# Kernel tuning notes

Hardware: AMD Instinct MI355X
Metric: run time of the kernel (lower is better)

Reference implementation:

```python
import jax, jax.numpy as jnp
import numpy as np

VOCAB = 32000
N = 4096        # reservoir_size
D = 32          # avg nonzeros per row -> density D/N
R_OUT = 512
BATCH = 8
T = 256
NNZ = N * D     # W_rec nonzeros = N*N*(D/N)


def setup_inputs() -> dict:
    key = jax.random.key(0)
    ks = jax.random.split(key, 9)
    x = jax.random.randint(ks[0], (BATCH, T), 0, VOCAB)
    # dense input table; sparse.mm(W_in_T, one_hot) == row gather W_in[x_t]
    W_in = jax.random.normal(ks[1], (VOCAB, N), jnp.float32)
    rec_rows = jax.random.randint(ks[2], (NNZ,), 0, N, dtype=jnp.int32)
    rec_cols = jax.random.randint(ks[3], (NNZ,), 0, N, dtype=jnp.int32)
    # small scale stands in for spectral-radius normalization (init-time detail)
    rec_vals = jax.random.normal(ks[4], (NNZ,), jnp.float32) * 0.05
    a = jax.random.uniform(ks[5], (N,), jnp.float32)  # leak rates in [0,1)
    B_w = jax.random.normal(ks[6], (R_OUT, N), jnp.float32) / np.sqrt(N)
    A_w = jax.random.normal(ks[7], (VOCAB, R_OUT), jnp.float32) / np.sqrt(R_OUT)
    A_b = jnp.zeros((VOCAB,), jnp.float32)
    return dict(x=x, W_in=W_in, rec_rows=rec_rows, rec_cols=rec_cols,
                rec_vals=rec_vals, a=a, B_w=B_w, A_w=A_w, A_b=A_b)


def reference(x, W_in, rec_rows, rec_cols, rec_vals, a, B_w, A_w, A_b):
    B = x.shape[0]

    def step(h, x_t):
        # input projection: one-hot @ W_in  ==  row gather
        u = W_in[x_t]                                   # (B, N)
        # sparse COO matvec: rec = W_rec @ h^T, batched over B
        contrib = rec_vals[None, :] * h[:, rec_cols]    # (B, nnz)
        rec = jnp.zeros_like(h).at[:, rec_rows].add(contrib)
        pre = jnp.clip(u + rec, -10.0, 10.0)
        h_new = (1.0 - a) * h + a * jnp.tanh(pre)
        out = (h_new @ B_w.T) @ A_w.T + A_b             # (B, vocab)
        return h_new, out

    h0 = jnp.zeros((B, W_in.shape[1]), W_in.dtype)
    _, outs = jax.lax.scan(step, h0, x.T)               # (T, B, V)
    return jnp.transpose(outs, (1, 0, 2))               # (B, T, V)
```

## Files before the change

### kernel.cpp

```cpp
#include <hip/hip_runtime.h>
#include <hip/hip_bf16.h>
#include <stdint.h>

#define N_RES 4096
#define BATCH 8
#define T_STEPS 256
#define VOCAB 32000
#define R_OUT 512
#define NNZ 131072
#define NNZ_CAP 163840
#define TEAMS 8
#define SLICES 16
#define ROWS_PS 256
#define NWG (TEAMS*SLICES)
#define CSR_CAP 10240

typedef _Float16 v8h __attribute__((ext_vector_type(8)));
typedef float v4f __attribute__((ext_vector_type(4)));

static __device__ __forceinline__ unsigned short f2h(float f) {
    _Float16 h = (_Float16)f;
    unsigned short u;
    __builtin_memcpy(&u, &h, 2);
    return u;
}
static __device__ __forceinline__ float h2f(unsigned short u) {
    _Float16 h;
    __builtin_memcpy(&h, &u, 2);
    return (float)h;
}


__global__ __launch_bounds__(256) void k_zero(unsigned* p, int n) {
    int i = blockIdx.x * 256 + threadIdx.x;
    if (i < n) p[i] = 0u;
}

__global__ __launch_bounds__(256) void k_hist(const int* __restrict__ rows,
                                              int* __restrict__ cnt) {
    int i = blockIdx.x * 256 + threadIdx.x;
    if (i < NNZ) atomicAdd(&cnt[rows[i]], 1);
}

__global__ __launch_bounds__(1024) void k_scan(const int* __restrict__ cnt,
                                               int* __restrict__ row_ptr,
                                               int* __restrict__ cursor) {
    __shared__ int sm[1024];
    int t = threadIdx.x;
    int base = t * 4;
    int c0 = (cnt[base] + 7) & ~7;
    int c1 = (cnt[base + 1] + 7) & ~7;
    int c2 = (cnt[base + 2] + 7) & ~7;
    int c3 = (cnt[base + 3] + 7) & ~7;
    int s = c0 + c1 + c2 + c3;
    sm[t] = s;
    __syncthreads();
    for (int off = 1; off < 1024; off <<= 1) {
        int v = (t >= off) ? sm[t - off] : 0;
        __syncthreads();
        sm[t] += v;
        __syncthreads();
    }
    int run = sm[t] - s;
    row_ptr[base] = run;     cursor[base] = run;     run += c0;
    row_ptr[base + 1] = run; cursor[base + 1] = run; run += c1;
    row_ptr[base + 2] = run; cursor[base + 2] = run; run += c2;
    row_ptr[base + 3] = run; cursor[base + 3] = run; run += c3;
    if (t == 1023) row_ptr[4096] = run;
}

__global__ __launch_bounds__(256) void k_fill(const int* __restrict__ rows,
                                              const int* __restrict__ cols,
                                              const float* __restrict__ vals,
                                              int* __restrict__ cursor,
                                              unsigned* __restrict__ csr) {
    int i = blockIdx.x * 256 + threadIdx.x;
    if (i < NNZ) {
        int r = rows[i];
        int c = cols[i];
        int p = atomicAdd(&cursor[r], 1);
        unsigned off = ((unsigned)(c & 15) << 10) | ((unsigned)(c >> 4) << 2);
        csr[p] = (off << 16) | (unsigned)f2h(vals[i]);
    }
}


__global__ __launch_bounds__(256) void k_cvt(const float* __restrict__ src,
                                             unsigned short* __restrict__ dst, int n) {
    int i = (blockIdx.x * 256 + threadIdx.x) * 8;
    if (i < n) {
        float4 a0 = *reinterpret_cast<const float4*>(src + i);
        float4 a1 = *reinterpret_cast<const float4*>(src + i + 4);
        unsigned short o[8] = { f2h(a0.x), f2h(a0.y), f2h(a0.z), f2h(a0.w),
                                f2h(a1.x), f2h(a1.y), f2h(a1.z), f2h(a1.w) };
        *reinterpret_cast<uint4*>(dst + i) = *reinterpret_cast<const uint4*>(o);
    }
}


__global__ __launch_bounds__(256) void k_steps(const int* __restrict__ rowptr,
                                               const unsigned* __restrict__ csr,
                                               const float* __restrict__ W_in,
                                               const int* __restrict__ x,
                                               const float* __restrict__ a,
                                               unsigned short* __restrict__ Hb,
                                               unsigned long long* __restrict__ hx,
                                               unsigned* __restrict__ flags) {
    __shared__ float plane[4096];
    __shared__ __align__(16) unsigned lcsr[CSR_CAP];
    __shared__ unsigned long long stage64[64];
    __shared__ int ltok[T_STEPS];

    int wg = blockIdx.x;
    int tid = threadIdx.x;
    int team = wg & 7;
    int slice = wg >> 3;
    int r_own = slice * ROWS_PS + tid;

    ltok[tid] = x[team * T_STEPS + tid];

    int j0 = rowptr[slice * ROWS_PS];
    int j1 = rowptr[slice * ROWS_PS + ROWS_PS];
    int cntE = j1 - j0;
    if (cntE > CSR_CAP) cntE = CSR_CAP;
    {
        const uint4* src = reinterpret_cast<const uint4*>(csr + j0);
        int n4 = cntE >> 2;
        for (int k = tid; k < n4; k += 256)
            reinterpret_cast<uint4*>(lcsr)[k] = src[k];
    }
    for (int k = tid; k < 4096; k += 256) plane[k] = 0.f;

    int js = rowptr[r_own] - j0;
    int je = rowptr[r_own + 1] - j0;
    if (js > CSR_CAP) js = CSR_CAP;
    if (je > CSR_CAP) je = CSR_CAP;
    float av = a[r_own];
    float oma = 1.f - av;
    int pown = ((r_own & 15) << 8) | (r_own >> 4);
    __syncthreads();

    float u_cur = W_in[(size_t)ltok[0] * N_RES + r_own];

    for (int t = 0; t < T_STEPS; ++t) {
        float u_nxt = 0.f;
        if (t + 1 < T_STEPS)
            u_nxt = W_in[(size_t)ltok[t + 1] * N_RES + r_own];

        float acc = 0.f;
        for (int j = js; j < je; j += 8) {
            uint4 e0 = *reinterpret_cast<const uint4*>(lcsr + j);
            uint4 e1 = *reinterpret_cast<const uint4*>(lcsr + j + 4);
            unsigned ee[8] = { e0.x, e0.y, e0.z, e0.w, e1.x, e1.y, e1.z, e1.w };
#pragma unroll
            for (int q = 0; q < 8; ++q) {
                float g = *reinterpret_cast<const float*>(
                    reinterpret_cast<const char*>(plane) + (ee[q] >> 16));
                acc += h2f((unsigned short)(ee[q] & 0xffffu)) * g;
            }
        }
        float hold = plane[pown];
        float pre = u_cur + acc;
        pre = fminf(fmaxf(pre, -10.f), 10.f);
        float ex = __expf(2.f * pre);
        float th = 1.f - 2.f / (ex + 1.f);
        float hv = oma * hold + av * th;
        unsigned short hv16 = f2h(hv);
        Hb[((size_t)(team * T_STEPS + t) << 12) + r_own] = hv16;
        u_cur = u_nxt;

        if (t == T_STEPS - 1) break;

        reinterpret_cast<unsigned short*>(stage64)[tid] = hv16;
        __syncthreads();
        int par = t & 1;
        unsigned long long* base = hx + ((size_t)(par * TEAMS + team)) * 1024;
        if (tid < 64) {
            unsigned long long d = stage64[tid];
            __hip_atomic_store(base + slice * 64 + tid, d,
                               __ATOMIC_RELAXED, __HIP_MEMORY_SCOPE_AGENT);
        }
        asm volatile("s_waitcnt vmcnt(0)" ::: "memory");
        __syncthreads();
        if (tid == 0)
            __hip_atomic_store(flags + (team * SLICES + slice) * 32, (unsigned)(t + 1),
                               __ATOMIC_RELAXED, __HIP_MEMORY_SCOPE_AGENT);
        if (tid < SLICES) {
            const unsigned* fp = flags + (team * SLICES + tid) * 32;
            while (__hip_atomic_load(fp, __ATOMIC_RELAXED,
                                     __HIP_MEMORY_SCOPE_AGENT) < (unsigned)(t + 1)) {}
        }
        __syncthreads();
        const unsigned long long* src = base + tid * 4;
#pragma unroll
        for (int k = 0; k < 4; ++k) {
            unsigned long long d = __hip_atomic_load(src + k, __ATOMIC_RELAXED,
                                                     __HIP_MEMORY_SCOPE_AGENT);
            int jb = k * 4;
            plane[((jb + 0) << 8) | tid] = h2f((unsigned short)(d & 0xffffu));
            plane[((jb + 1) << 8) | tid] = h2f((unsigned short)((d >> 16) & 0xffffu));
            plane[((jb + 2) << 8) | tid] = h2f((unsigned short)((d >> 32) & 0xffffu));
            plane[((jb + 3) << 8) | tid] = h2f((unsigned short)((d >> 48) & 0xffffu));
        }
        __syncthreads();
    }
}


__global__ __launch_bounds__(512) void k_gemm1(const unsigned short* __restrict__ Hb,
                                               const unsigned short* __restrict__ Bwh,
                                               unsigned short* __restrict__ Rbh) {
    int lane = threadIdx.x & 63, wave = threadIdx.x >> 6;
    int wm = wave >> 1, wn = wave & 1;
    int row0 = blockIdx.y * 128;
    int col0 = blockIdx.x * 128 + wn * 64;
    int rA = lane & 15, kA = (lane >> 4) * 8;
    v4f acc[2][4];
    for (int s = 0; s < 2; ++s)
        for (int f = 0; f < 4; ++f)
            acc[s][f] = (v4f){0.f, 0.f, 0.f, 0.f};

    for (int k0 = 0; k0 < N_RES; k0 += 32) {
        v8h af[2];
#pragma unroll
        for (int s = 0; s < 2; ++s) {
            int r = row0 + (wm * 2 + s) * 16 + rA;
            af[s] = *reinterpret_cast<const v8h*>(Hb + (size_t)r * N_RES + k0 + kA);
        }
        v8h bf[4];
#pragma unroll
        for (int f = 0; f < 4; ++f) {
            int c = col0 + f * 16 + rA;
            bf[f] = *reinterpret_cast<const v8h*>(Bwh + (size_t)c * N_RES + k0 + kA);
        }
#pragma unroll
        for (int s = 0; s < 2; ++s)
#pragma unroll
            for (int f = 0; f < 4; ++f)
                acc[s][f] = __builtin_amdgcn_mfma_f32_16x16x32_f16(af[s], bf[f], acc[s][f], 0, 0, 0);
    }
#pragma unroll
    for (int s = 0; s < 2; ++s)
#pragma unroll
        for (int f = 0; f < 4; ++f) {
            int col = col0 + f * 16 + (lane & 15);
#pragma unroll
            for (int r = 0; r < 4; ++r) {
                int row = row0 + (wm * 2 + s) * 16 + (lane >> 4) * 4 + r;
                Rbh[(size_t)row * R_OUT + col] = f2h(acc[s][f][r]);
            }
        }
}


__global__ __launch_bounds__(512) void k_gemm2(const unsigned short* __restrict__ Rbh,
                                               const unsigned short* __restrict__ Awh,
                                               const float* __restrict__ Ab,
                                               float* __restrict__ out) {
    int lane = threadIdx.x & 63, wave = threadIdx.x >> 6;
    int wm = wave >> 1, wn = wave & 1;
    int row0 = blockIdx.x * 256;
    int col0 = blockIdx.y * 128 + wn * 64;
    int rA = lane & 15, kA = (lane >> 4) * 8;
    v4f acc[4][4];
    for (int s = 0; s < 4; ++s)
        for (int f = 0; f < 4; ++f)
            acc[s][f] = (v4f){0.f, 0.f, 0.f, 0.f};

    for (int k0 = 0; k0 < R_OUT; k0 += 32) {
        v8h af[4];
#pragma unroll
        for (int s = 0; s < 4; ++s) {
            int r = row0 + (wm * 4 + s) * 16 + rA;
            af[s] = *reinterpret_cast<const v8h*>(Rbh + (size_t)r * R_OUT + k0 + kA);
        }
        v8h bf[4];
#pragma unroll
        for (int f = 0; f < 4; ++f) {
            int c = col0 + f * 16 + rA;
            bf[f] = *reinterpret_cast<const v8h*>(Awh + (size_t)c * R_OUT + k0 + kA);
        }
#pragma unroll
        for (int s = 0; s < 4; ++s)
#pragma unroll
            for (int f = 0; f < 4; ++f)
                acc[s][f] = __builtin_amdgcn_mfma_f32_16x16x32_f16(af[s], bf[f], acc[s][f], 0, 0, 0);
    }
#pragma unroll
    for (int f = 0; f < 4; ++f) {
        int col = col0 + f * 16 + (lane & 15);
        float bias = Ab[col];
#pragma unroll
        for (int s = 0; s < 4; ++s) {
#pragma unroll
            for (int r = 0; r < 4; ++r) {
                int row = row0 + (wm * 4 + s) * 16 + (lane >> 4) * 4 + r;
                out[(size_t)row * VOCAB + col] = acc[s][f][r] + bias;
            }
        }
    }
}


extern "C" void kernel_launch(void* const* d_in, const int* in_sizes, int n_in,
                              void* d_out, int out_size, void* d_ws, size_t ws_size,
                              hipStream_t stream) {
    const int*   x        = (const int*)d_in[0];
    const float* W_in     = (const float*)d_in[1];
    const int*   rec_rows = (const int*)d_in[2];
    const int*   rec_cols = (const int*)d_in[3];
    const float* rec_vals = (const float*)d_in[4];
    const float* a        = (const float*)d_in[5];
    const float* B_w      = (const float*)d_in[6];
    const float* A_w      = (const float*)d_in[7];
    const float* A_b      = (const float*)d_in[8];
    float* out = (float*)d_out;

    char* w = (char*)d_ws;
    size_t off = 0;
    auto alloc = [&](size_t bytes) { void* p = w + off; off = (off + bytes + 255) & ~(size_t)255; return p; };

    unsigned short* Hb     = (unsigned short*)alloc((size_t)2048 * N_RES * 2);
    unsigned short* Rbh    = (unsigned short*)alloc((size_t)2048 * R_OUT * 2);
    unsigned short* Bwh    = (unsigned short*)alloc((size_t)R_OUT * N_RES * 2);
    unsigned short* Awh    = (unsigned short*)alloc((size_t)VOCAB * R_OUT * 2);
    unsigned*       csr    = (unsigned*)alloc((size_t)NNZ_CAP * 4);
    int*            rowptr = (int*)alloc(4097 * 4);
    int*            cnt    = (int*)alloc(4096 * 4);
    int*            cursor = (int*)alloc(4096 * 4);
    unsigned long long* hx = (unsigned long long*)alloc(2 * TEAMS * 1024 * 8);
    unsigned*       flags  = (unsigned*)alloc(TEAMS * SLICES * 32 * 4);

    k_zero<<<(NNZ_CAP + 255) / 256, 256, 0, stream>>>(csr, NNZ_CAP);
    k_zero<<<16, 256, 0, stream>>>((unsigned*)cnt, 4096);
    k_zero<<<16, 256, 0, stream>>>(flags, TEAMS * SLICES * 32);

    k_hist<<<(NNZ + 255) / 256, 256, 0, stream>>>(rec_rows, cnt);
    k_scan<<<1, 1024, 0, stream>>>(cnt, rowptr, cursor);
    k_fill<<<(NNZ + 255) / 256, 256, 0, stream>>>(rec_rows, rec_cols, rec_vals, cursor, csr);

    k_cvt<<<(R_OUT * N_RES / 8 + 255) / 256, 256, 0, stream>>>(B_w, Bwh, R_OUT * N_RES);
    k_cvt<<<(VOCAB * R_OUT / 8 + 255) / 256, 256, 0, stream>>>(A_w, Awh, VOCAB * R_OUT);

    k_steps<<<NWG, 256, 0, stream>>>(rowptr, csr, W_in, x, a, Hb, hx, flags);

    k_gemm1<<<dim3(R_OUT / 128, 2048 / 128), 512, 0, stream>>>(Hb, Bwh, Rbh);
    k_gemm2<<<dim3(2048 / 256, VOCAB / 128), 512, 0, stream>>>(Rbh, Awh, A_b, out);
}
```

Measured before the change: 1.501 ms.

## Replace flag barrier with epoch-tagged per-element exchange words in recurrent steps

Each thread now publishes its new hidden value as a 32-bit word carrying the step epoch in the upper half, written directly to a double-buffered global exchange array. Each thread then spins on its own 16 input words until all carry the current epoch. This removes the shared staging, the store drain, the per-slice flag stores and flag polling, and two workgroup barriers per step. In exchange, every thread polls 16 scattered global words instead of a few threads polling flags, which adds memory traffic during the spin. The exchange buffer is zero-initialized so the epoch tags start clean.

```diff
diff --git a/kernel.cpp b/kernel.cpp
--- a/kernel.cpp
+++ b/kernel.cpp
@@ -104,11 +104,9 @@
                                                const int* __restrict__ x,
                                                const float* __restrict__ a,
                                                unsigned short* __restrict__ Hb,
-                                               unsigned long long* __restrict__ hx,
-                                               unsigned* __restrict__ flags) {
+                                               unsigned* __restrict__ hx) {
     __shared__ float plane[4096];
     __shared__ __align__(16) unsigned lcsr[CSR_CAP];
-    __shared__ unsigned long long stage64[64];
     __shared__ int ltok[T_STEPS];
 
     int wg = blockIdx.x;
@@ -138,6 +136,7 @@
     float av = a[r_own];
     float oma = 1.f - av;
     int pown = ((r_own & 15) << 8) | (r_own >> 4);
+    int rbase = tid * 16;
     __syncthreads();
 
     float u_cur = W_in[(size_t)ltok[0] * N_RES + r_own];
@@ -166,42 +165,41 @@
         float th = 1.f - 2.f / (ex + 1.f);
         float hv = oma * hold + av * th;
         unsigned short hv16 = f2h(hv);
+        u_cur = u_nxt;
+
+        unsigned e = (unsigned)(t + 1);
+        int par = (int)(e & 1u);
+        unsigned* xbase = hx + (((size_t)par * TEAMS + team) << 12);
+
+        if (t < T_STEPS - 1) {
+            __hip_atomic_store(xbase + r_own, (e << 16) | (unsigned)hv16,
+                               __ATOMIC_RELAXED, __HIP_MEMORY_SCOPE_AGENT);
+        }
         Hb[((size_t)(team * T_STEPS + t) << 12) + r_own] = hv16;
-        u_cur = u_nxt;
 
         if (t == T_STEPS - 1) break;
 
-        reinterpret_cast<unsigned short*>(stage64)[tid] = hv16;
+        unsigned got[16];
+#pragma unroll
+        for (int k = 0; k < 16; ++k)
+            got[k] = __hip_atomic_load(xbase + rbase + k,
+                                       __ATOMIC_RELAXED, __HIP_MEMORY_SCOPE_AGENT);
+        for (;;) {
+            unsigned m = 0;
+#pragma unroll
+            for (int k = 0; k < 16; ++k)
+                m |= ((got[k] >> 16) != e) ? (1u << k) : 0u;
+            if (!m) break;
+#pragma unroll
+            for (int k = 0; k < 16; ++k)
+                if (m & (1u << k))
+                    got[k] = __hip_atomic_load(xbase + rbase + k,
+                                               __ATOMIC_RELAXED, __HIP_MEMORY_SCOPE_AGENT);
+        }
         __syncthreads();
-        int par = t & 1;
-        unsigned long long* base = hx + ((size_t)(par * TEAMS + team)) * 1024;
-        if (tid < 64) {
-            unsigned long long d = stage64[tid];
-            __hip_atomic_store(base + slice * 64 + tid, d,
-                               __ATOMIC_RELAXED, __HIP_MEMORY_SCOPE_AGENT);
-        }
-        asm volatile("s_waitcnt vmcnt(0)" ::: "memory");
-        __syncthreads();
-        if (tid == 0)
-            __hip_atomic_store(flags + (team * SLICES + slice) * 32, (unsigned)(t + 1),
-                               __ATOMIC_RELAXED, __HIP_MEMORY_SCOPE_AGENT);
-        if (tid < SLICES) {
-            const unsigned* fp = flags + (team * SLICES + tid) * 32;
-            while (__hip_atomic_load(fp, __ATOMIC_RELAXED,
-                                     __HIP_MEMORY_SCOPE_AGENT) < (unsigned)(t + 1)) {}
-        }
-        __syncthreads();
-        const unsigned long long* src = base + tid * 4;
-#pragma unroll
-        for (int k = 0; k < 4; ++k) {
-            unsigned long long d = __hip_atomic_load(src + k, __ATOMIC_RELAXED,
-                                                     __HIP_MEMORY_SCOPE_AGENT);
-            int jb = k * 4;
-            plane[((jb + 0) << 8) | tid] = h2f((unsigned short)(d & 0xffffu));
-            plane[((jb + 1) << 8) | tid] = h2f((unsigned short)((d >> 16) & 0xffffu));
-            plane[((jb + 2) << 8) | tid] = h2f((unsigned short)((d >> 32) & 0xffffu));
-            plane[((jb + 3) << 8) | tid] = h2f((unsigned short)((d >> 48) & 0xffffu));
-        }
+#pragma unroll
+        for (int k = 0; k < 16; ++k)
+            plane[(k << 8) | tid] = h2f((unsigned short)(got[k] & 0xffffu));
         __syncthreads();
     }
 }
@@ -328,12 +326,11 @@
     int*            rowptr = (int*)alloc(4097 * 4);
     int*            cnt    = (int*)alloc(4096 * 4);
     int*            cursor = (int*)alloc(4096 * 4);
-    unsigned long long* hx = (unsigned long long*)alloc(2 * TEAMS * 1024 * 8);
-    unsigned*       flags  = (unsigned*)alloc(TEAMS * SLICES * 32 * 4);
+    unsigned*       hx     = (unsigned*)alloc((size_t)2 * TEAMS * 4096 * 4);
 
     k_zero<<<(NNZ_CAP + 255) / 256, 256, 0, stream>>>(csr, NNZ_CAP);
     k_zero<<<16, 256, 0, stream>>>((unsigned*)cnt, 4096);
-    k_zero<<<16, 256, 0, stream>>>(flags, TEAMS * SLICES * 32);
+    k_zero<<<(2 * TEAMS * 4096 + 255) / 256, 256, 0, stream>>>(hx, 2 * TEAMS * 4096);
 
     k_hist<<<(NNZ + 255) / 256, 256, 0, stream>>>(rec_rows, cnt);
     k_scan<<<1, 1024, 0, stream>>>(cnt, rowptr, cursor);
@@ -342,7 +339,7 @@
     k_cvt<<<(R_OUT * N_RES / 8 + 255) / 256, 256, 0, stream>>>(B_w, Bwh, R_OUT * N_RES);
     k_cvt<<<(VOCAB * R_OUT / 8 + 255) / 256, 256, 0, stream>>>(A_w, Awh, VOCAB * R_OUT);
 
-    k_steps<<<NWG, 256, 0, stream>>>(rowptr, csr, W_in, x, a, Hb, hx, flags);
+    k_steps<<<NWG, 256, 0, stream>>>(rowptr, csr, W_in, x, a, Hb, hx);
 
     k_gemm1<<<dim3(R_OUT / 128, 2048 / 128), 512, 0, stream>>>(Hb, Bwh, Rbh);
     k_gemm2<<<dim3(2048 / 256, VOCAB / 128), 512, 0, stream>>>(Rbh, Awh, A_b, out);
```

After: 2.076 ms. +38.2%, slower.
